# Kernel tuning notes

Hardware: AMD Instinct MI355X
Metric: run time of the kernel (lower is better)

## Reference

```python
import jax, jax.numpy as jnp
import numpy as np

B, S, V, E, H = 4096, 64, 100000, 128, 128

_PARAM_NAMES = ["Wz", "Uzl", "Uzr", "Wr", "Url", "Urr", "Wh", "Uhl", "Uhr"]


def setup_inputs() -> dict:
    key = jax.random.key(0)
    ks = jax.random.split(key, 2 + 2 * len(_PARAM_NAMES))
    inp = {"tokens": jax.random.randint(ks[0], (B, S), 0, V)}
    inp["emb"] = jax.random.normal(ks[1], (V, E), jnp.float32)
    i = 2
    for n in _PARAM_NAMES:
        din = E if n.startswith("W") else H
        inp[n] = jax.random.normal(ks[i], (din, H), jnp.float32) / np.sqrt(din).astype(np.float32)
        i += 1
        inp["b" + n] = jax.random.normal(ks[i], (H,), jnp.float32) * 0.01
        i += 1
    return inp


def _tree_gru(word, hl, hr, p):
    # word: [..., E], hl/hr: [..., H]
    z = jax.nn.sigmoid(word @ p["Wz"] + p["bWz"] + hl @ p["Uzl"] + p["bUzl"] + hr @ p["Uzr"] + p["bUzr"])
    r = jax.nn.sigmoid(word @ p["Wr"] + p["bWr"] + hl @ p["Url"] + p["bUrl"] + hr @ p["Urr"] + p["bUrr"])
    h_tilde = jnp.tanh(word @ p["Wh"] + p["bWh"] + (r * hl) @ p["Uhl"] + p["bUhl"] + (r * hr) @ p["Uhr"] + p["bUhr"])
    return z * hl + z * hr + (1.0 - z) * h_tilde


def reference(tokens, emb, Wz, bWz, Uzl, bUzl, Uzr, bUzr, Wr, bWr, Url, bUrl, Urr, bUrr, Wh, bWh, Uhl, bUhl, Uhr, bUhr):
    p = dict(Wz=Wz, bWz=bWz, Uzl=Uzl, bUzl=bUzl, Uzr=Uzr, bUzr=bUzr,
             Wr=Wr, bWr=bWr, Url=Url, bUrl=bUrl, Urr=Urr, bUrr=bUrr,
             Wh=Wh, bWh=bWh, Uhl=Uhl, bUhl=bUhl, Uhr=Uhr, bUhr=bUhr)
    x = emb[tokens]                                   # [B, S, E]
    h0 = jnp.zeros(x.shape[:2] + (H,), x.dtype)
    cur = _tree_gru(x, h0, h0, p)                     # leaf nodes [B, S, H]
    n = cur.shape[1]
    while n > 1:                                      # static loop over log2(S) tree levels
        left, right = cur[:, 0::2], cur[:, 1::2]      # pair adjacent nodes
        word0 = jnp.zeros(left.shape[:2] + (E,), cur.dtype)
        cur = _tree_gru(word0, left, right, p)
        n //= 2
    return cur.transpose(1, 0, 2)                     # [1, B, H] (matches torch transpose(0,1))
```

## Files before the change

kernel.cpp:

```cpp
#include <hip/hip_runtime.h>


typedef _Float16 half_t;
typedef __attribute__((ext_vector_type(8))) _Float16 f16x8;
typedef __attribute__((ext_vector_type(4))) float f32x4;

#define NTOK 262144
#define NB 4096
#define NV 100000
#define C1 1.4426950408889634f
#define C2 2.8853900817779268f
#define LS 272

__device__ __forceinline__ float sigm2(float x){
  return __builtin_amdgcn_rcpf(1.0f + __builtin_amdgcn_exp2f(-x));
}
__device__ __forceinline__ float tanh2(float y){
  float r = __builtin_amdgcn_rcpf(1.0f + __builtin_amdgcn_exp2f(y));
  return __builtin_fmaf(-2.0f, r, 1.0f);
}

__global__ __launch_bounds__(256) void wprep_k(
    const float* Wz, const float* Wh,
    const float* Uzl,const float* Uzr,const float* Url,const float* Urr,
    const float* Uhl,const float* Uhr,
    const float* bWz,const float* bUzl,const float* bUzr,
    const float* bWr,const float* bUrl,const float* bUrr,
    const float* bWh,const float* bUhl,const float* bUhr,
    half_t* wb, float* bc){
  int idx = blockIdx.x*256 + threadIdx.x;
  if (idx < 32768){
    const float* W = (idx < 16384) ? Wz : Wh;
    float sc = (idx < 16384) ? C1 : C2;
    int t = idx & 16383;
    int w = t >> 11, ks = (t >> 9) & 3, l = (t >> 3) & 63, j = t & 7;
    int n = w*16 + (l & 15);
    int k = ks*32 + ((l >> 4) << 3) + j;
    wb[idx] = (half_t)(W[k*128 + n] * sc);
  } else {
    int t = idx - 32768;
    int mat = t >> 15;
    t &= 32767;
    int w = t >> 12, ks = (t >> 9) & 7, l = (t >> 3) & 63, j = t & 7;
    int n = w*16 + (l & 15);
    int kp = ks*32 + ((l >> 4) << 3) + j;
    int k = kp >> 1;
    const float* U;
    if (mat == 0) U = (kp & 1) ? Uzr : Uzl;
    else if (mat == 1) U = (kp & 1) ? Urr : Url;
    else U = (kp & 1) ? Uhr : Uhl;
    float sc = (mat == 2) ? C2 : C1;
    wb[idx] = (half_t)(U[k*128 + n] * sc);
  }
  if (blockIdx.x == 511 && threadIdx.x < 128){
    int j = threadIdx.x;
    bc[j]       = (bWz[j] + bUzl[j] + bUzr[j]) * C1;
    bc[128 + j] = (bWr[j] + bUrl[j] + bUrr[j]) * C1;
    bc[256 + j] = (bWh[j] + bUhl[j] + bUhr[j]) * C2;
  }
}

template<int MT>
__global__ __launch_bounds__(512, 8) void h1tab_k(
    const float* __restrict__ emb,
    const half_t* __restrict__ Wz_f, const half_t* __restrict__ Wh_f,
    const float* __restrict__ bc, half_t* __restrict__ t1)
{
  __shared__ __align__(16) _Float16 xs[MT*16][144];
  const int tid = threadIdx.x;
  const int m0  = blockIdx.x*(MT*16);
  #pragma unroll
  for (int it = 0; it < MT; it++){
    int idx = it*512 + tid;
    int m = idx >> 5, c = idx & 31;
    int row = m0 + m; if (row >= NV) row = 0;
    float4 v = ((const float4*)(emb + (size_t)row*128))[c];
    union { half_t h[4]; ushort4 u; } p;
    p.h[0]=(half_t)v.x; p.h[1]=(half_t)v.y; p.h[2]=(half_t)v.z; p.h[3]=(half_t)v.w;
    *(ushort4*)&xs[m][c*4] = p.u;
  }
  __syncthreads();
  const int w = tid>>6, l = tid&63;
  const int lr = l&15, lk = (l>>4)*8, lq = (l>>4)*4;
  const int col = w*16 + lr;

  f32x4 zacc[MT] = {}; f32x4 hacc[MT] = {};
  const half_t* wzp = Wz_f + ((w*4)*64 + l)*8;
  const half_t* whp = Wh_f + ((w*4)*64 + l)*8;
  #pragma unroll
  for (int ks=0; ks<4; ks++){
    f16x8 bz = *(const f16x8*)(wzp + ks*512);
    f16x8 bh = *(const f16x8*)(whp + ks*512);
    #pragma unroll
    for (int mt=0; mt<MT; mt++){
      f16x8 a = *(const f16x8*)&xs[mt*16 + lr][ks*32 + lk];
      zacc[mt] = __builtin_amdgcn_mfma_f32_16x16x32_f16(a, bz, zacc[mt],0,0,0);
      hacc[mt] = __builtin_amdgcn_mfma_f32_16x16x32_f16(a, bh, hacc[mt],0,0,0);
    }
  }
  const float bzv = bc[col], bhv = bc[256+col];
  #pragma unroll
  for (int mt=0; mt<MT; mt++){
    #pragma unroll
    for (int q=0; q<4; q++){
      int row = m0 + mt*16 + lq + q;
      if (row < NV){
        float z  = sigm2(zacc[mt][q] + bzv);
        float ht = tanh2(hacc[mt][q] + bhv);
        t1[(size_t)row*128 + col] = (half_t)((1.f-z)*ht);
      }
    }
  }
}

template<int MT, int RV, int LAST>
static __device__ __forceinline__ void level_step(
    _Float16 (*X)[LS], _Float16 (*Y)[LS], int tid,
    const half_t* Uz_f, const half_t* Ur_f, const half_t* Uh_f,
    const float* bc, float* outf, int outrow0, int slot0)
{
  const int w = tid>>6, l = tid&63;
  const int lr = l&15, lk = (l>>4)*8, lq = (l>>4)*4;
  const int col = w*16 + lr;

  f32x4 zacc[MT] = {}, racc[MT] = {};
  const half_t* uzp = Uz_f + ((w*8)*64 + l)*8;
  const half_t* urp = Ur_f + ((w*8)*64 + l)*8;
  #pragma unroll
  for (int ks=0; ks<8; ks++){
    f16x8 bz = *(const f16x8*)(uzp + ks*512);
    f16x8 br = *(const f16x8*)(urp + ks*512);
    #pragma unroll
    for (int mt=0; mt<MT; mt++){
      f16x8 a = *(const f16x8*)&X[mt*16 + lr][ks*32 + lk];
      zacc[mt] = __builtin_amdgcn_mfma_f32_16x16x32_f16(a, bz, zacc[mt],0,0,0);
      racc[mt] = __builtin_amdgcn_mfma_f32_16x16x32_f16(a, br, racc[mt],0,0,0);
    }
  }
  __syncthreads();

  uint zp[MT][2], sp[MT][2];
  const float bzv = bc[col], brv = bc[128+col];
  #pragma unroll
  for (int mt=0; mt<MT; mt++){
    union { half_t h[4]; uint u[2]; } pz, ps;
    #pragma unroll
    for (int q=0; q<4; q++){
      int row = mt*16 + lq + q;
      union { uint u; half_t h[2]; } io;
      io.u = *(uint*)&X[row][2*col];
      float hl = (float)io.h[0];
      float hr = (float)io.h[1];
      float z  = sigm2(zacc[mt][q] + bzv);
      float rv = sigm2(racc[mt][q] + brv);
      pz.h[q] = (half_t)z;
      ps.h[q] = (half_t)(hl + hr);
      io.h[0] = (half_t)(rv*hl);
      io.h[1] = (half_t)(rv*hr);
      *(uint*)&X[row][2*col] = io.u;
    }
    zp[mt][0]=pz.u[0]; zp[mt][1]=pz.u[1];
    sp[mt][0]=ps.u[0]; sp[mt][1]=ps.u[1];
  }
  __syncthreads();

  f32x4 ha[MT] = {};
  const half_t* uhp = Uh_f + ((w*8)*64 + l)*8;
  #pragma unroll
  for (int ks=0; ks<8; ks++){
    f16x8 bh = *(const f16x8*)(uhp + ks*512);
    #pragma unroll
    for (int mt=0; mt<MT; mt++){
      f16x8 a = *(const f16x8*)&X[mt*16 + lr][ks*32 + lk];
      ha[mt] = __builtin_amdgcn_mfma_f32_16x16x32_f16(a, bh, ha[mt],0,0,0);
    }
  }
  const float bhv = bc[256+col];
  #pragma unroll
  for (int mt=0; mt<MT; mt++){
    union { half_t h[4]; uint u[2]; } pz, ps;
    pz.u[0]=zp[mt][0]; pz.u[1]=zp[mt][1];
    ps.u[0]=sp[mt][0]; ps.u[1]=sp[mt][1];
    #pragma unroll
    for (int q=0; q<4; q++){
      int row = mt*16 + lq + q;
      if (row < RV){
        float ht = tanh2(ha[mt][q] + bhv);
        float z  = (float)pz.h[q];
        float o  = z*(float)ps.h[q] + (1.f-z)*ht;
        if (LAST) outf[(size_t)(outrow0 + row)*128 + col] = o;
        else      Y[slot0 + (row>>1)][2*col + (row&1)] = (half_t)o;
      }
    }
  }
  __syncthreads();
}

__global__ __launch_bounds__(512, 2) void fused_k(
    const half_t* __restrict__ t1, const int* __restrict__ tokens,
    float* __restrict__ outf,
    const half_t* __restrict__ Uz_f, const half_t* __restrict__ Ur_f, const half_t* __restrict__ Uh_f,
    const float* __restrict__ bc)
{
  __shared__ __align__(16) _Float16 XA[64][LS];
  __shared__ __align__(16) _Float16 XB[64][LS];
  const int tid = threadIdx.x;
  const int g = blockIdx.x;

  uint2 sA[2][4], sB[2][4];
  auto gload = [&](int k){
    #pragma unroll
    for (int it = 0; it < 4; it++){
      int idx = it*512 + tid;
      int m = idx >> 5, c = idx & 31;
      int gm = 128*g + 64*k + m;
      int tl = tokens[2*gm], tr = tokens[2*gm+1];
      sA[k][it] = *(const uint2*)(t1 + (size_t)tl*128 + c*4);
      sB[k][it] = *(const uint2*)(t1 + (size_t)tr*128 + c*4);
    }
  };
  auto gwrite = [&](int k){
    #pragma unroll
    for (int it = 0; it < 4; it++){
      int idx = it*512 + tid;
      int m = idx >> 5, c = idx & 31;
      uint2 A = sA[k][it], Bv = sB[k][it];
      uint4 o;
      o.x = (A.x & 0xFFFFu) | (Bv.x << 16);
      o.y = (A.x >> 16)     | (Bv.x & 0xFFFF0000u);
      o.z = (A.y & 0xFFFFu) | (Bv.y << 16);
      o.w = (A.y >> 16)     | (Bv.y & 0xFFFF0000u);
      *(uint4*)&XA[m][c*8] = o;
    }
  };

  gload(0);
  gwrite(0);
  gload(1);
  __syncthreads();
  level_step<4,64,0>(XA, XB, tid, Uz_f, Ur_f, Uh_f, bc, outf, 0, 0);
  gwrite(1);
  __syncthreads();
  level_step<4,64,0>(XA, XB, tid, Uz_f, Ur_f, Uh_f, bc, outf, 0, 32);

  level_step<4,64,0>(XB, XA, tid, Uz_f, Ur_f, Uh_f, bc, outf, 0, 0);
  level_step<2,32,0>(XA, XB, tid, Uz_f, Ur_f, Uh_f, bc, outf, 0, 0);
  level_step<1,16,0>(XB, XA, tid, Uz_f, Ur_f, Uh_f, bc, outf, 0, 0);
  level_step<1, 8,0>(XA, XB, tid, Uz_f, Ur_f, Uh_f, bc, outf, 0, 0);
  level_step<1, 4,1>(XB, XA, tid, Uz_f, Ur_f, Uh_f, bc, outf, 4*g, 0);
}

extern "C" void kernel_launch(void* const* d_in, const int* in_sizes, int n_in,
                              void* d_out, int out_size, void* d_ws, size_t ws_size,
                              hipStream_t stream) {
  const int*   tokens = (const int*)  d_in[0];
  const float* emb    = (const float*)d_in[1];
  const float* Wz  = (const float*)d_in[2];  const float* bWz  = (const float*)d_in[3];
  const float* Uzl = (const float*)d_in[4];  const float* bUzl = (const float*)d_in[5];
  const float* Uzr = (const float*)d_in[6];  const float* bUzr = (const float*)d_in[7];
  const float* Wr  = (const float*)d_in[8];  const float* bWr  = (const float*)d_in[9];
  const float* Url = (const float*)d_in[10]; const float* bUrl = (const float*)d_in[11];
  const float* Urr = (const float*)d_in[12]; const float* bUrr = (const float*)d_in[13];
  const float* Wh  = (const float*)d_in[14]; const float* bWh  = (const float*)d_in[15];
  const float* Uhl = (const float*)d_in[16]; const float* bUhl = (const float*)d_in[17];
  const float* Uhr = (const float*)d_in[18]; const float* bUhr = (const float*)d_in[19];

  float*  bc = (float*)d_ws;
  half_t* wb = (half_t*)((char*)d_ws + 4096);
  half_t* Wz_f = wb;
  half_t* Wh_f = wb + 16384;
  half_t* Uz_f = wb + 32768;
  half_t* Ur_f = wb + 65536;
  half_t* Uh_f = wb + 98304;
  half_t* t1 = (half_t*)((char*)d_ws + (1<<20));

  wprep_k<<<512, 256, 0, stream>>>(Wz,Wh,Uzl,Uzr,Url,Urr,Uhl,Uhr,
                                   bWz,bUzl,bUzr,bWr,bUrl,bUrr,bWh,bUhl,bUhr, wb, bc);

  h1tab_k<4><<<(NV + 63)/64, 512, 0, stream>>>(emb, Wz_f, Wh_f, bc, t1);

  fused_k<<<1024, 512, 0, stream>>>(t1, tokens, (float*)d_out, Uz_f, Ur_f, Uh_f, bc);
}
```

Baseline: 128.4 us.

## Shrink fused kernel LDS footprint with aliased buffer slots and raise occupancy

Replaces the two 64-row shared buffers with one 96-row buffer. Each level's input is split into two 32-row halves so outputs can overwrite rows that are already consumed, with an extra barrier where output aliases input. The launch bounds minimum-blocks hint goes from 2 to 6, aiming for more resident blocks per CU to hide gather and MFMA latency. This adds per-tile pointer selection and tighter register pressure, and correctness relies on the aliasing schedule staying race-free.

```diff
diff --git a/kernel.cpp b/kernel.cpp
--- a/kernel.cpp
+++ b/kernel.cpp
@@ -113,11 +113,11 @@
   }
 }
 
-template<int MT, int RV, int LAST>
+template<int MT, int RV, int LAST, int SYNCB>
 static __device__ __forceinline__ void level_step(
-    _Float16 (*X)[LS], _Float16 (*Y)[LS], int tid,
+    _Float16 (*XL)[LS], _Float16 (*XH)[LS], _Float16 (*Y)[LS], int tid,
     const half_t* Uz_f, const half_t* Ur_f, const half_t* Uh_f,
-    const float* bc, float* outf, int outrow0, int slot0)
+    const float* bc, float* outf, int outrow0)
 {
   const int w = tid>>6, l = tid&63;
   const int lr = l&15, lk = (l>>4)*8, lq = (l>>4)*4;
@@ -132,7 +132,9 @@
     f16x8 br = *(const f16x8*)(urp + ks*512);
     #pragma unroll
     for (int mt=0; mt<MT; mt++){
-      f16x8 a = *(const f16x8*)&X[mt*16 + lr][ks*32 + lk];
+      _Float16 (*Xr)[LS] = (MT==4 && mt>=2) ? XH : XL;
+      int rb = (MT==4 && mt>=2) ? (mt-2)*16 : mt*16;
+      f16x8 a = *(const f16x8*)&Xr[rb + lr][ks*32 + lk];
       zacc[mt] = __builtin_amdgcn_mfma_f32_16x16x32_f16(a, bz, zacc[mt],0,0,0);
       racc[mt] = __builtin_amdgcn_mfma_f32_16x16x32_f16(a, br, racc[mt],0,0,0);
     }
@@ -143,12 +145,14 @@
   const float bzv = bc[col], brv = bc[128+col];
   #pragma unroll
   for (int mt=0; mt<MT; mt++){
+    _Float16 (*Xr)[LS] = (MT==4 && mt>=2) ? XH : XL;
+    int rb = (MT==4 && mt>=2) ? (mt-2)*16 : mt*16;
     union { half_t h[4]; uint u[2]; } pz, ps;
     #pragma unroll
     for (int q=0; q<4; q++){
-      int row = mt*16 + lq + q;
+      int row = rb + lq + q;
       union { uint u; half_t h[2]; } io;
-      io.u = *(uint*)&X[row][2*col];
+      io.u = *(uint*)&Xr[row][2*col];
       float hl = (float)io.h[0];
       float hr = (float)io.h[1];
       float z  = sigm2(zacc[mt][q] + bzv);
@@ -157,7 +161,7 @@
       ps.h[q] = (half_t)(hl + hr);
       io.h[0] = (half_t)(rv*hl);
       io.h[1] = (half_t)(rv*hr);
-      *(uint*)&X[row][2*col] = io.u;
+      *(uint*)&Xr[row][2*col] = io.u;
     }
     zp[mt][0]=pz.u[0]; zp[mt][1]=pz.u[1];
     sp[mt][0]=ps.u[0]; sp[mt][1]=ps.u[1];
@@ -171,10 +175,13 @@
     f16x8 bh = *(const f16x8*)(uhp + ks*512);
     #pragma unroll
     for (int mt=0; mt<MT; mt++){
-      f16x8 a = *(const f16x8*)&X[mt*16 + lr][ks*32 + lk];
+      _Float16 (*Xr)[LS] = (MT==4 && mt>=2) ? XH : XL;
+      int rb = (MT==4 && mt>=2) ? (mt-2)*16 : mt*16;
+      f16x8 a = *(const f16x8*)&Xr[rb + lr][ks*32 + lk];
       ha[mt] = __builtin_amdgcn_mfma_f32_16x16x32_f16(a, bh, ha[mt],0,0,0);
     }
   }
+  if (SYNCB) __syncthreads();
   const float bhv = bc[256+col];
   #pragma unroll
   for (int mt=0; mt<MT; mt++){
@@ -189,21 +196,20 @@
         float z  = (float)pz.h[q];
         float o  = z*(float)ps.h[q] + (1.f-z)*ht;
         if (LAST) outf[(size_t)(outrow0 + row)*128 + col] = o;
-        else      Y[slot0 + (row>>1)][2*col + (row&1)] = (half_t)o;
+        else      Y[row>>1][2*col + (row&1)] = (half_t)o;
       }
     }
   }
   __syncthreads();
 }
 
-__global__ __launch_bounds__(512, 2) void fused_k(
+__global__ __launch_bounds__(512, 6) void fused_k(
     const half_t* __restrict__ t1, const int* __restrict__ tokens,
     float* __restrict__ outf,
     const half_t* __restrict__ Uz_f, const half_t* __restrict__ Ur_f, const half_t* __restrict__ Uh_f,
     const float* __restrict__ bc)
 {
-  __shared__ __align__(16) _Float16 XA[64][LS];
-  __shared__ __align__(16) _Float16 XB[64][LS];
+  __shared__ __align__(16) _Float16 X[96][LS];
   const int tid = threadIdx.x;
   const int g = blockIdx.x;
 
@@ -230,7 +236,7 @@
       o.y = (A.x >> 16)     | (Bv.x & 0xFFFF0000u);
       o.z = (A.y & 0xFFFFu) | (Bv.y << 16);
       o.w = (A.y >> 16)     | (Bv.y & 0xFFFF0000u);
-      *(uint4*)&XA[m][c*8] = o;
+      *(uint4*)&X[m][c*8] = o;
     }
   };
 
@@ -238,16 +244,16 @@
   gwrite(0);
   gload(1);
   __syncthreads();
-  level_step<4,64,0>(XA, XB, tid, Uz_f, Ur_f, Uh_f, bc, outf, 0, 0);
+  level_step<4,64,0,0>(&X[0], &X[32], &X[64], tid, Uz_f, Ur_f, Uh_f, bc, outf, 0);
   gwrite(1);
   __syncthreads();
-  level_step<4,64,0>(XA, XB, tid, Uz_f, Ur_f, Uh_f, bc, outf, 0, 32);
-
-  level_step<4,64,0>(XB, XA, tid, Uz_f, Ur_f, Uh_f, bc, outf, 0, 0);
-  level_step<2,32,0>(XA, XB, tid, Uz_f, Ur_f, Uh_f, bc, outf, 0, 0);
-  level_step<1,16,0>(XB, XA, tid, Uz_f, Ur_f, Uh_f, bc, outf, 0, 0);
-  level_step<1, 8,0>(XA, XB, tid, Uz_f, Ur_f, Uh_f, bc, outf, 0, 0);
-  level_step<1, 4,1>(XB, XA, tid, Uz_f, Ur_f, Uh_f, bc, outf, 4*g, 0);
+  level_step<4,64,0,1>(&X[0], &X[32], &X[0],  tid, Uz_f, Ur_f, Uh_f, bc, outf, 0);
+
+  level_step<4,64,0,0>(&X[64], &X[0], &X[32], tid, Uz_f, Ur_f, Uh_f, bc, outf, 0);
+  level_step<2,32,0,0>(&X[32], &X[32], &X[0], tid, Uz_f, Ur_f, Uh_f, bc, outf, 0);
+  level_step<1,16,0,0>(&X[0],  &X[0],  &X[16],tid, Uz_f, Ur_f, Uh_f, bc, outf, 0);
+  level_step<1, 8,0,0>(&X[16], &X[16], &X[0], tid, Uz_f, Ur_f, Uh_f, bc, outf, 0);
+  level_step<1, 4,1,0>(&X[0],  &X[0],  &X[0], tid, Uz_f, Ur_f, Uh_f, bc, outf, 4*g);
 }
 
 extern "C" void kernel_launch(void* const* d_in, const int* in_sizes, int n_in,
```

Result: no change. 128.9 us (+0.4%).

## Software-pipeline embedding table kernel: two 64-row tiles per block with prefetch

Applied to the files above, without the earlier changes.

The leaf-table kernel now handles 128 embedding rows per block as two 64-row tiles. The global load of the second tile is issued before computing the first, so the memory latency overlaps the MFMA and activation work, and the block count is halved. The cost is higher register use for the staged float4 values and LDS doubled to two buffers, which may lower occupancy.

```diff
diff --git a/kernel.cpp b/kernel.cpp
--- a/kernel.cpp
+++ b/kernel.cpp
@@ -60,57 +60,77 @@
   }
 }
 
-template<int MT>
 __global__ __launch_bounds__(512, 8) void h1tab_k(
     const float* __restrict__ emb,
     const half_t* __restrict__ Wz_f, const half_t* __restrict__ Wh_f,
     const float* __restrict__ bc, half_t* __restrict__ t1)
 {
-  __shared__ __align__(16) _Float16 xs[MT*16][144];
+  __shared__ __align__(16) _Float16 xs[2][64][144];
   const int tid = threadIdx.x;
-  const int m0  = blockIdx.x*(MT*16);
-  #pragma unroll
-  for (int it = 0; it < MT; it++){
-    int idx = it*512 + tid;
-    int m = idx >> 5, c = idx & 31;
-    int row = m0 + m; if (row >= NV) row = 0;
-    float4 v = ((const float4*)(emb + (size_t)row*128))[c];
-    union { half_t h[4]; ushort4 u; } p;
-    p.h[0]=(half_t)v.x; p.h[1]=(half_t)v.y; p.h[2]=(half_t)v.z; p.h[3]=(half_t)v.w;
-    *(ushort4*)&xs[m][c*4] = p.u;
-  }
-  __syncthreads();
+  const int m0  = blockIdx.x*128;
   const int w = tid>>6, l = tid&63;
   const int lr = l&15, lk = (l>>4)*8, lq = (l>>4)*4;
   const int col = w*16 + lr;
-
-  f32x4 zacc[MT] = {}; f32x4 hacc[MT] = {};
+  const float bzv = bc[col], bhv = bc[256+col];
   const half_t* wzp = Wz_f + ((w*4)*64 + l)*8;
   const half_t* whp = Wh_f + ((w*4)*64 + l)*8;
-  #pragma unroll
-  for (int ks=0; ks<4; ks++){
-    f16x8 bz = *(const f16x8*)(wzp + ks*512);
-    f16x8 bh = *(const f16x8*)(whp + ks*512);
-    #pragma unroll
-    for (int mt=0; mt<MT; mt++){
-      f16x8 a = *(const f16x8*)&xs[mt*16 + lr][ks*32 + lk];
-      zacc[mt] = __builtin_amdgcn_mfma_f32_16x16x32_f16(a, bz, zacc[mt],0,0,0);
-      hacc[mt] = __builtin_amdgcn_mfma_f32_16x16x32_f16(a, bh, hacc[mt],0,0,0);
-    }
-  }
-  const float bzv = bc[col], bhv = bc[256+col];
-  #pragma unroll
-  for (int mt=0; mt<MT; mt++){
-    #pragma unroll
-    for (int q=0; q<4; q++){
-      int row = m0 + mt*16 + lq + q;
-      if (row < NV){
-        float z  = sigm2(zacc[mt][q] + bzv);
-        float ht = tanh2(hacc[mt][q] + bhv);
-        t1[(size_t)row*128 + col] = (half_t)((1.f-z)*ht);
+
+  float4 stg[2][4];
+  auto gload = [&](int t){
+    #pragma unroll
+    for (int it = 0; it < 4; it++){
+      int idx = it*512 + tid;
+      int m = idx >> 5, c = idx & 31;
+      int row = m0 + t*64 + m; if (row >= NV) row = 0;
+      stg[t][it] = ((const float4*)(emb + (size_t)row*128))[c];
+    }
+  };
+  auto gwrite = [&](int t){
+    #pragma unroll
+    for (int it = 0; it < 4; it++){
+      int idx = it*512 + tid;
+      int m = idx >> 5, c = idx & 31;
+      float4 v = stg[t][it];
+      union { half_t h[4]; ushort4 u; } p;
+      p.h[0]=(half_t)v.x; p.h[1]=(half_t)v.y; p.h[2]=(half_t)v.z; p.h[3]=(half_t)v.w;
+      *(ushort4*)&xs[t][m][c*4] = p.u;
+    }
+  };
+  auto compute = [&](int t){
+    f32x4 zacc[4] = {}; f32x4 hacc[4] = {};
+    #pragma unroll
+    for (int ks=0; ks<4; ks++){
+      f16x8 bz = *(const f16x8*)(wzp + ks*512);
+      f16x8 bh = *(const f16x8*)(whp + ks*512);
+      #pragma unroll
+      for (int mt=0; mt<4; mt++){
+        f16x8 a = *(const f16x8*)&xs[t][mt*16 + lr][ks*32 + lk];
+        zacc[mt] = __builtin_amdgcn_mfma_f32_16x16x32_f16(a, bz, zacc[mt],0,0,0);
+        hacc[mt] = __builtin_amdgcn_mfma_f32_16x16x32_f16(a, bh, hacc[mt],0,0,0);
       }
     }
-  }
+    #pragma unroll
+    for (int mt=0; mt<4; mt++){
+      #pragma unroll
+      for (int q=0; q<4; q++){
+        int row = m0 + t*64 + mt*16 + lq + q;
+        if (row < NV){
+          float z  = sigm2(zacc[mt][q] + bzv);
+          float ht = tanh2(hacc[mt][q] + bhv);
+          t1[(size_t)row*128 + col] = (half_t)((1.f-z)*ht);
+        }
+      }
+    }
+  };
+
+  gload(0);
+  gwrite(0);
+  gload(1);
+  __syncthreads();
+  compute(0);
+  gwrite(1);
+  __syncthreads();
+  compute(1);
 }
 
 template<int MT, int RV, int LAST>
@@ -277,7 +297,7 @@
   wprep_k<<<512, 256, 0, stream>>>(Wz,Wh,Uzl,Uzr,Url,Urr,Uhl,Uhr,
                                    bWz,bUzl,bUzr,bWr,bUrl,bUrr,bWh,bUhl,bUhr, wb, bc);
 
-  h1tab_k<4><<<(NV + 63)/64, 512, 0, stream>>>(emb, Wz_f, Wh_f, bc, t1);
+  h1tab_k<<<(NV + 127)/128, 512, 0, stream>>>(emb, Wz_f, Wh_f, bc, t1);
 
   fused_k<<<1024, 512, 0, stream>>>(t1, tokens, (float*)d_out, Uz_f, Ur_f, Uh_f, bc);
 }
```

Result: slower. 154.2 us (+20.1%).
